# Performance work log

Measured on AMD Instinct MI355X. Metric: run time of the kernel, lower is better.

## Reference

```python
import jax, jax.numpy as jnp
import numpy as np

D_MODEL = 1024
HEADS = 16
D_K = D_MODEL // HEADS

def setup_inputs() -> dict:
    key = jax.random.key(0)
    ks = jax.random.split(key, 12)
    B, S = 4, 2048
    sc = 1.0 / np.sqrt(D_MODEL)
    inp = {
        'q': jax.random.normal(ks[0], (B, S, D_MODEL), jnp.float32),
        'k': jax.random.normal(ks[1], (B, S, D_MODEL), jnp.float32),
        'v': jax.random.normal(ks[2], (B, S, D_MODEL), jnp.float32),
        'mask': jnp.ones((B, S, S), jnp.int32),
        'Wq': jax.random.normal(ks[3], (D_MODEL, D_MODEL), jnp.float32) * sc,
        'bq': jnp.zeros((D_MODEL,), jnp.float32),
        'Wk': jax.random.normal(ks[4], (D_MODEL, D_MODEL), jnp.float32) * sc,
        'bk': jnp.zeros((D_MODEL,), jnp.float32),
        'Wv': jax.random.normal(ks[5], (D_MODEL, D_MODEL), jnp.float32) * sc,
        'bv': jnp.zeros((D_MODEL,), jnp.float32),
        'Wo': jax.random.normal(ks[6], (D_MODEL, D_MODEL), jnp.float32) * sc,
        'bo': jnp.zeros((D_MODEL,), jnp.float32),
    }
    return inp

def _proj_heads(x, W, b):
    # torch Linear: y = x @ W.T + b; then view(B,S,h,dk).transpose(1,2) -> [B,h,S,dk]
    B, S, _ = x.shape
    y = jnp.einsum('bsd,ed->bse', x, W) + b
    return y.reshape(B, S, HEADS, D_K).transpose(0, 2, 1, 3)

def reference(q, k, v, mask, Wq, bq, Wk, bk, Wv, bv, Wo, bo):
    B, S, _ = q.shape
    qh = _proj_heads(q, Wq, bq)  # [B,h,S,dk]
    kh = _proj_heads(k, Wk, bk)
    vh = _proj_heads(v, Wv, bv)
    scores = jnp.einsum('bhqd,bhkd->bhqk', qh, kh) / np.sqrt(D_K)
    scores = jnp.where(mask[:, None, :, :] == 0, jnp.float32(-1e9), scores)
    probs = jax.nn.softmax(scores, axis=-1)  # dropout = identity (eval mode)
    ctx = jnp.einsum('bhqk,bhkd->bhqd', probs, vh)
    concat = ctx.transpose(0, 2, 1, 3).reshape(B, S, D_MODEL)
    return jnp.einsum('bsd,ed->bse', concat, Wo) + bo
```

## Files before the change

kernel.cpp:

```cpp
#include <hip/hip_runtime.h>
#include <stdint.h>

#define DM 1024
#define SQL 2048
#define NB 4
#define NH 16
#define DK 64

typedef unsigned short u16;
typedef unsigned int u32;
typedef float f32x4 __attribute__((ext_vector_type(4)));
typedef short s16x8 __attribute__((ext_vector_type(8)));
typedef unsigned int u32x2 __attribute__((ext_vector_type(2)));

__device__ __forceinline__ u16 f2bf(float x) {
  union { float f; u32 u; } un; un.f = x;
  return (u16)((un.u + 0x8000u) >> 16);
}
__device__ __forceinline__ u32 pack_bf16(float a, float b) {
  return (u32)f2bf(a) | ((u32)f2bf(b) << 16);
}

typedef __attribute__((address_space(3))) u32 lds_u32_t;
typedef __attribute__((address_space(1))) u32 g_u32_t;

__device__ __forceinline__ void async_cp16(void* lds, const void* g) {
  __builtin_amdgcn_global_load_lds((g_u32_t*)(unsigned long long)g,
                                   (lds_u32_t*)(unsigned long long)lds,
                                   16, 0, 0);
}

__device__ __forceinline__ void mfma16(f32x4& c, s16x8 a, s16x8 b) {
  c = __builtin_amdgcn_mfma_f32_16x16x32_bf16(a, b, c, 0, 0, 0);
}

__global__ void init_flag_k(int* flag) { if (threadIdx.x == 0) *flag = 1; }

__device__ __forceinline__ void store_bf4(u16* dst, float4 v) {
  u32 lo = pack_bf16(v.x, v.y);
  u32 hi = pack_bf16(v.z, v.w);
  ((u32*)dst)[0] = lo; ((u32*)dst)[1] = hi;
}

__global__ void __launch_bounds__(256) convert_scan_k(
    const float* __restrict__ q, const float* __restrict__ k, const float* __restrict__ v,
    const float* __restrict__ wq, const float* __restrict__ wk,
    const float* __restrict__ wv, const float* __restrict__ wo,
    const int* __restrict__ mask,
    u16* qb, u16* kb, u16* vb, u16* wqb, u16* wkb, u16* wvb, u16* wob, int* flag)
{
  const size_t i = (size_t)blockIdx.x * 256 + threadIdx.x;
  const size_t i4 = i * 4;
  store_bf4(qb + i4, *(const float4*)(q + i4));
  store_bf4(kb + i4, *(const float4*)(k + i4));
  store_bf4(vb + i4, *(const float4*)(v + i4));
  if (i4 < 1048576) {
    store_bf4(wqb + i4, *(const float4*)(wq + i4));
    store_bf4(wkb + i4, *(const float4*)(wk + i4));
    store_bf4(wvb + i4, *(const float4*)(wv + i4));
    store_bf4(wob + i4, *(const float4*)(wo + i4));
  }
  const size_t mi = i * 8;
  int4 m0 = *(const int4*)(mask + mi);
  int4 m1 = *(const int4*)(mask + mi + 4);
  bool z = (m0.x == 0) | (m0.y == 0) | (m0.z == 0) | (m0.w == 0) |
           (m1.x == 0) | (m1.y == 0) | (m1.z == 0) | (m1.w == 0);
  if (z) *flag = 0;
}

__device__ __forceinline__ void gemm_core(const u16* __restrict__ A, const u16* __restrict__ W,
                                          int m0, int n0, u16* sA, u16* sB, f32x4 (&acc)[4][4])
{
  const int tid = threadIdx.x;
  const int l = tid & 63, w = tid >> 6;
  const int g = l >> 4, ln = l & 15;
  const int wm = w & 1, wn = w >> 1;

  for (int kt = 0; kt < DM; kt += 64) {
#pragma unroll
    for (int i = 0; i < 4; ++i) {
      int s = w * 256 + i * 64 + l;
      int m = s >> 3;
      int kc = (s & 7) ^ (m & 7);
      async_cp16(sA + (size_t)(w * 256 + i * 64) * 8,
                 A + (size_t)(m0 + m) * DM + kt + kc * 8);
    }
#pragma unroll
    for (int i = 0; i < 4; ++i) {
      int s = w * 256 + i * 64 + l;
      int n = s >> 3;
      int kc = (s & 7) ^ (n & 7);
      async_cp16(sB + (size_t)(w * 256 + i * 64) * 8,
                 W + (size_t)(n0 + n) * DM + kt + kc * 8);
    }
    asm volatile("s_waitcnt vmcnt(0)" ::: "memory");
    __syncthreads();
#pragma unroll
    for (int ks = 0; ks < 2; ++ks) {
      s16x8 af[4], bfr[4];
#pragma unroll
      for (int mt = 0; mt < 4; ++mt) {
        int m = wm * 64 + mt * 16 + ln;
        int slot = m * 8 + ((ks * 4 + g) ^ (m & 7));
        af[mt] = *(const s16x8*)(sA + (size_t)slot * 8);
      }
#pragma unroll
      for (int nt = 0; nt < 4; ++nt) {
        int n = wn * 64 + nt * 16 + ln;
        int slot = n * 8 + ((ks * 4 + g) ^ (n & 7));
        bfr[nt] = *(const s16x8*)(sB + (size_t)slot * 8);
      }
#pragma unroll
      for (int mt = 0; mt < 4; ++mt)
#pragma unroll
        for (int nt = 0; nt < 4; ++nt)
          mfma16(acc[mt][nt], af[mt], bfr[nt]);
    }
    __syncthreads();
  }
}

__global__ void __launch_bounds__(256) gemm_qkv_k(
    const u16* __restrict__ qb, const u16* __restrict__ kb, const u16* __restrict__ vb,
    const u16* __restrict__ wqb, const u16* __restrict__ wkb, const u16* __restrict__ wvb,
    const float* __restrict__ bq, const float* __restrict__ bk, const float* __restrict__ bv,
    u16* Qh, u16* Kh, u16* Vt)
{
  __shared__ __align__(16) u16 sA[128 * 64];
  __shared__ __align__(16) u16 sB[128 * 64];
  const int z = blockIdx.z;
  const u16* A = (z == 0) ? qb : ((z == 1) ? kb : vb);
  const u16* W = (z == 0) ? wqb : ((z == 1) ? wkb : wvb);
  const float* bias = (z == 0) ? bq : ((z == 1) ? bk : bv);
  const int m0 = blockIdx.y * 128, n0 = blockIdx.x * 128;

  f32x4 zero4 = {0.f, 0.f, 0.f, 0.f};
  f32x4 acc[4][4];
#pragma unroll
  for (int mt = 0; mt < 4; ++mt)
#pragma unroll
    for (int nt = 0; nt < 4; ++nt) acc[mt][nt] = zero4;

  gemm_core(A, W, m0, n0, sA, sB, acc);

  const int tid = threadIdx.x;
  const int l = tid & 63, w = tid >> 6, g = l >> 4, ln = l & 15;
  const int wm = w & 1, wn = w >> 1;
  const float scale = (z == 0) ? (0.125f * 1.44269504089f) : 1.0f;
  u16* Crow = (z == 0) ? Qh : Kh;
#pragma unroll
  for (int nt = 0; nt < 4; ++nt) {
    int n = n0 + wn * 64 + nt * 16 + ln;
    float bn = bias[n];
#pragma unroll
    for (int mt = 0; mt < 4; ++mt) {
      int mb = m0 + wm * 64 + mt * 16 + g * 4;
      f32x4 vv = acc[mt][nt];
      if (z < 2) {
#pragma unroll
        for (int r = 0; r < 4; ++r)
          Crow[(size_t)(mb + r) * DM + n] = f2bf((vv[r] + bn) * scale);
      } else {
        int b = mb >> 11, s = mb & 2047;
        u32 lo = pack_bf16(vv[0] + bn, vv[1] + bn);
        u32 hi = pack_bf16(vv[2] + bn, vv[3] + bn);
        u32* dst = (u32*)(Vt + ((size_t)b << 21) + (size_t)n * SQL + s);
        dst[0] = lo; dst[1] = hi;
      }
    }
  }
}

__device__ __forceinline__ void stage_kv(u16* Ks, u16* Vs,
                                         const u16* __restrict__ Kh,
                                         const u16* __restrict__ Vt,
                                         int b, int h, int kv0, int w, int l) {
#pragma unroll
  for (int i = 0; i < 4; ++i) {
    int s = w * 256 + i * 64 + l;
    int m = s >> 3;
    int kc = (s & 7) ^ (m & 7);
    async_cp16(Ks + (size_t)(w * 256 + i * 64) * 8,
               Kh + (size_t)(b * SQL + kv0 + m) * DM + h * DK + kc * 8);
  }
#pragma unroll
  for (int i = 0; i < 4; ++i) {
    int s = w * 256 + i * 64 + l;
    int d = s >> 4;
    int kc = (s & 15) ^ (d & 15);
    async_cp16(Vs + (size_t)(w * 256 + i * 64) * 8,
               Vt + ((size_t)b << 21) + (size_t)(h * DK + d) * SQL + kv0 + kc * 8);
  }
}

__device__ __forceinline__ s16x8 p_transpose(u32 x0, u32 x1, u32 y0, u32 y1,
                                             const int LA, const int LB, bool ghi) {
  union { u32 wds[4]; s16x8 v; } pu;
#if __has_builtin(__builtin_amdgcn_permlane32_swap) && __has_builtin(__builtin_amdgcn_permlane16_swap)
  u32x2 r0 = __builtin_amdgcn_permlane32_swap(x0, y0, false, false);
  u32x2 s0 = __builtin_amdgcn_permlane16_swap(r0.x, r0.y, false, false);
  u32x2 r1 = __builtin_amdgcn_permlane32_swap(x1, y1, false, false);
  u32x2 s1 = __builtin_amdgcn_permlane16_swap(r1.x, r1.y, false, false);
  pu.wds[0] = s0.x; pu.wds[1] = s1.x; pu.wds[2] = s0.y; pu.wds[3] = s1.y;
#else
  u32 a0 = __shfl(x0, LA, 64), a1 = __shfl(x1, LA, 64);
  u32 b0 = __shfl(x0, LB, 64), b1 = __shfl(x1, LB, 64);
  u32 c0 = __shfl(y0, LA, 64), c1 = __shfl(y1, LA, 64);
  u32 d0 = __shfl(y0, LB, 64), d1 = __shfl(y1, LB, 64);
  pu.wds[0] = ghi ? c0 : a0;
  pu.wds[1] = ghi ? c1 : a1;
  pu.wds[2] = ghi ? d0 : b0;
  pu.wds[3] = ghi ? d1 : b1;
#endif
  return pu.v;
}

__global__ void __launch_bounds__(256, 2) attn_k(
    const u16* __restrict__ Qh, const u16* __restrict__ Kh, const u16* __restrict__ Vt,
    const int* __restrict__ mask, const int* __restrict__ flag, u16* __restrict__ ctx)
{
  __shared__ __align__(16) u16 smem[32768];
  const int tid = threadIdx.x;
  const int l = tid & 63, w = tid >> 6, g = l >> 4, ln = l & 15;
  const int wq = w >> 1, wk = w & 1;
  const int flat = blockIdx.x + 16 * (blockIdx.y + 16 * blockIdx.z);
  const int nid = (flat & 7) * 128 + (flat >> 3);
  const int q0 = (nid & 15) * 128;
  const int bh = nid >> 4;
  const int h = bh & 15, b = bh >> 4;
  const int allones = *flag;

  s16x8 qf[4][2];
#pragma unroll
  for (int u = 0; u < 4; ++u)
#pragma unroll
    for (int ks = 0; ks < 2; ++ks) {
      size_t row = (size_t)(b * SQL + q0 + wq * 64 + u * 16 + ln);
      qf[u][ks] = *(const s16x8*)(Qh + row * DM + h * DK + ks * 32 + g * 8);
    }

  f32x4 zero4 = {0.f, 0.f, 0.f, 0.f};
  f32x4 ot[4][4];
#pragma unroll
  for (int mt = 0; mt < 4; ++mt)
#pragma unroll
    for (int u = 0; u < 4; ++u) ot[mt][u] = zero4;
  float lsum[4] = {0.f, 0.f, 0.f, 0.f};

  const int LA = (g & 1) * 32 + ln;
  const int LB = LA + 16;
  const bool ghi = (g >> 1) != 0;

  stage_kv(smem, smem + 8192, Kh, Vt, b, h, 0, w, l);

  for (int t = 0; t < 16; ++t) {
    const int kv0 = t * 128;
    u16* Ks = smem + (t & 1) * 16384;
    u16* Vs = smem + 8192 + (t & 1) * 16384;
    if (t < 15) {
      stage_kv(smem + ((t + 1) & 1) * 16384, smem + 8192 + ((t + 1) & 1) * 16384,
               Kh, Vt, b, h, kv0 + 128, w, l);
      asm volatile("s_waitcnt vmcnt(8)" ::: "memory");
    } else {
      asm volatile("s_waitcnt vmcnt(0)" ::: "memory");
    }
    asm volatile("s_barrier" ::: "memory");

#pragma unroll
    for (int kc = 0; kc < 2; ++kc) {
      f32x4 st[2][4];
#pragma unroll
      for (int t2 = 0; t2 < 2; ++t2)
#pragma unroll
        for (int u = 0; u < 4; ++u) st[t2][u] = zero4;
#pragma unroll
      for (int ks = 0; ks < 2; ++ks) {
#pragma unroll
        for (int t2 = 0; t2 < 2; ++t2) {
          int m = wk * 64 + (kc * 2 + t2) * 16 + ln;
          int slot = m * 8 + ((ks * 4 + g) ^ (m & 7));
          s16x8 kf = *(const s16x8*)(Ks + (size_t)slot * 8);
#pragma unroll
          for (int u = 0; u < 4; ++u) mfma16(st[t2][u], kf, qf[u][ks]);
        }
      }

      if (!allones) {
        const int* mb_ = mask + (size_t)b * SQL * SQL;
#pragma unroll
        for (int t2 = 0; t2 < 2; ++t2)
#pragma unroll
          for (int u = 0; u < 4; ++u)
#pragma unroll
            for (int r = 0; r < 4; ++r) {
              int kv = kv0 + wk * 64 + (kc * 2 + t2) * 16 + g * 4 + r;
              int qq = q0 + wq * 64 + u * 16 + ln;
              if (mb_[(size_t)qq * SQL + kv] == 0) st[t2][u][r] = -30.f;
            }
      }

#pragma unroll
      for (int u = 0; u < 4; ++u) {
        u32 pkw[2][2];
#pragma unroll
        for (int t2 = 0; t2 < 2; ++t2) {
          float p0 = __builtin_amdgcn_exp2f(st[t2][u][0]);
          float p1 = __builtin_amdgcn_exp2f(st[t2][u][1]);
          float p2 = __builtin_amdgcn_exp2f(st[t2][u][2]);
          float p3 = __builtin_amdgcn_exp2f(st[t2][u][3]);
          lsum[u] += (p0 + p1) + (p2 + p3);
          pkw[t2][0] = pack_bf16(p0, p1);
          pkw[t2][1] = pack_bf16(p2, p3);
        }
        s16x8 pf = p_transpose(pkw[0][0], pkw[0][1], pkw[1][0], pkw[1][1], LA, LB, ghi);
#pragma unroll
        for (int mt = 0; mt < 4; ++mt) {
          int d = mt * 16 + ln;
          int slot = d * 16 + ((wk * 8 + kc * 4 + g) ^ (d & 15));
          s16x8 vf = *(const s16x8*)(Vs + (size_t)slot * 8);
          mfma16(ot[mt][u], vf, pf);
        }
      }
    }

    asm volatile("s_waitcnt lgkmcnt(0)" ::: "memory");
    asm volatile("s_barrier" ::: "memory");
  }

#pragma unroll
  for (int u = 0; u < 4; ++u) {
    lsum[u] += __shfl_xor(lsum[u], 16, 64);
    lsum[u] += __shfl_xor(lsum[u], 32, 64);
  }

  float* red = (float*)smem;
  __syncthreads();
  if (wk == 1) {
#pragma unroll
    for (int u = 0; u < 4; ++u) {
      int row = wq * 64 + u * 16 + ln;
#pragma unroll
      for (int mt = 0; mt < 4; ++mt)
        *(f32x4*)&red[(size_t)row * 68 + mt * 16 + g * 4] = ot[mt][u];
      if (g == 0) red[(size_t)row * 68 + 64] = lsum[u];
    }
  }
  __syncthreads();
  if (wk == 0) {
#pragma unroll
    for (int u = 0; u < 4; ++u) {
      int row = wq * 64 + u * 16 + ln;
#pragma unroll
      for (int mt = 0; mt < 4; ++mt)
        ot[mt][u] += *(const f32x4*)&red[(size_t)row * 68 + mt * 16 + g * 4];
      lsum[u] += red[(size_t)row * 68 + 64];
    }
  }
  __syncthreads();
  if (wk == 0) {
#pragma unroll
    for (int u = 0; u < 4; ++u) {
      float inv = 1.0f / lsum[u];
      int row = wq * 64 + u * 16 + ln;
#pragma unroll
      for (int mt = 0; mt < 4; ++mt)
#pragma unroll
        for (int r = 0; r < 4; ++r)
          red[(size_t)row * 68 + mt * 16 + g * 4 + r] = ot[mt][u][r] * inv;
    }
  }
  __syncthreads();
#pragma unroll
  for (int i = 0; i < 16; ++i) {
    int f2 = i * 256 + tid;
    int qq = f2 >> 5, dp = f2 & 31;
    float2 vv = *(const float2*)&red[(size_t)qq * 68 + dp * 2];
    u32 pkd = pack_bf16(vv.x, vv.y);
    *(u32*)(ctx + (size_t)(b * SQL + q0 + qq) * DM + h * DK + dp * 2) = pkd;
  }
}

__global__ void __launch_bounds__(256) gemm_out_k(
    const u16* __restrict__ ctx, const u16* __restrict__ wob,
    const float* __restrict__ bo, float* __restrict__ out)
{
  __shared__ __align__(16) u16 sA[128 * 64];
  __shared__ __align__(16) u16 sB[128 * 64];
  const int m0 = blockIdx.y * 128, n0 = blockIdx.x * 128;
  f32x4 zero4 = {0.f, 0.f, 0.f, 0.f};
  f32x4 acc[4][4];
#pragma unroll
  for (int mt = 0; mt < 4; ++mt)
#pragma unroll
    for (int nt = 0; nt < 4; ++nt) acc[mt][nt] = zero4;

  gemm_core(ctx, wob, m0, n0, sA, sB, acc);

  const int tid = threadIdx.x;
  const int l = tid & 63, w = tid >> 6, g = l >> 4, ln = l & 15;
  const int wm = w & 1, wn = w >> 1;
#pragma unroll
  for (int nt = 0; nt < 4; ++nt) {
    int n = n0 + wn * 64 + nt * 16 + ln;
    float bn = bo[n];
#pragma unroll
    for (int mt = 0; mt < 4; ++mt) {
      int mb = m0 + wm * 64 + mt * 16 + g * 4;
      f32x4 vv = acc[mt][nt];
#pragma unroll
      for (int r = 0; r < 4; ++r)
        out[(size_t)(mb + r) * DM + n] = vv[r] + bn;
    }
  }
}

extern "C" void kernel_launch(void* const* d_in, const int* in_sizes, int n_in,
                              void* d_out, int out_size, void* d_ws, size_t ws_size,
                              hipStream_t stream) {
  (void)in_sizes; (void)n_in; (void)out_size; (void)ws_size;
  const float* q  = (const float*)d_in[0];
  const float* k  = (const float*)d_in[1];
  const float* v  = (const float*)d_in[2];
  const int* mask = (const int*)d_in[3];
  const float* Wq = (const float*)d_in[4];
  const float* bq = (const float*)d_in[5];
  const float* Wk = (const float*)d_in[6];
  const float* bk = (const float*)d_in[7];
  const float* Wv = (const float*)d_in[8];
  const float* bv = (const float*)d_in[9];
  const float* Wo = (const float*)d_in[10];
  const float* bo = (const float*)d_in[11];
  float* out = (float*)d_out;
  char* ws = (char*)d_ws;

  u16* qb  = (u16*)(ws + 0);
  u16* kb  = (u16*)(ws + 16777216);
  u16* vb  = (u16*)(ws + 33554432);
  u16* Qh  = (u16*)(ws + 50331648);
  u16* Kh  = (u16*)(ws + 67108864);
  u16* Vt  = (u16*)(ws + 83886080);
  u16* ctx = (u16*)(ws + 100663296);
  u16* wqb = (u16*)(ws + 117440512);
  u16* wkb = (u16*)(ws + 119537664);
  u16* wvb = (u16*)(ws + 121634816);
  u16* wob = (u16*)(ws + 123731968);
  int* flag = (int*)(ws + 125829120);

  hipLaunchKernelGGL(init_flag_k, dim3(1), dim3(64), 0, stream, flag);
  hipLaunchKernelGGL(convert_scan_k, dim3(8192), dim3(256), 0, stream,
                     q, k, v, Wq, Wk, Wv, Wo, mask,
                     qb, kb, vb, wqb, wkb, wvb, wob, flag);
  hipLaunchKernelGGL(gemm_qkv_k, dim3(8, 64, 3), dim3(256), 0, stream,
                     qb, kb, vb, wqb, wkb, wvb, bq, bk, bv, Qh, Kh, Vt);
  hipLaunchKernelGGL(attn_k, dim3(16, 16, 4), dim3(256), 0, stream,
                     Qh, Kh, Vt, mask, flag, ctx);
  hipLaunchKernelGGL(gemm_out_k, dim3(8, 64), dim3(256), 0, stream,
                     ctx, wob, bo, out);
}
```

Measured before the change: 404.6 us.

## Shrink attention KV tile to 64 and drop split-KV warp reduction

The attention kernel now stages 64-key K/V tiles instead of 128 and gives each of the four warps 32 distinct query rows, so warps no longer split the key range. This removes the end-of-kernel cross-warp LDS reduction of partial outputs and sums, and halves per-warp accumulator registers and LDS use so launch bounds can request 4 blocks per CU. The cost is twice as many loop iterations with a full __syncthreads each, and a simpler wait scheme (full barrier instead of vmcnt-based partial waits) that may expose more load latency.

```diff
diff --git a/kernel.cpp b/kernel.cpp
--- a/kernel.cpp
+++ b/kernel.cpp
@@ -176,19 +176,19 @@
                                          const u16* __restrict__ Vt,
                                          int b, int h, int kv0, int w, int l) {
 #pragma unroll
-  for (int i = 0; i < 4; ++i) {
-    int s = w * 256 + i * 64 + l;
+  for (int i = 0; i < 2; ++i) {
+    int s = w * 128 + i * 64 + l;
     int m = s >> 3;
     int kc = (s & 7) ^ (m & 7);
-    async_cp16(Ks + (size_t)(w * 256 + i * 64) * 8,
+    async_cp16(Ks + (size_t)(w * 128 + i * 64) * 8,
                Kh + (size_t)(b * SQL + kv0 + m) * DM + h * DK + kc * 8);
   }
 #pragma unroll
-  for (int i = 0; i < 4; ++i) {
-    int s = w * 256 + i * 64 + l;
-    int d = s >> 4;
-    int kc = (s & 15) ^ (d & 15);
-    async_cp16(Vs + (size_t)(w * 256 + i * 64) * 8,
+  for (int i = 0; i < 2; ++i) {
+    int s = w * 128 + i * 64 + l;
+    int d = s >> 3;
+    int kc = (s & 7) ^ (d & 7);
+    async_cp16(Vs + (size_t)(w * 128 + i * 64) * 8,
                Vt + ((size_t)b << 21) + (size_t)(h * DK + d) * SQL + kv0 + kc * 8);
   }
 }
@@ -215,14 +215,13 @@
   return pu.v;
 }
 
-__global__ void __launch_bounds__(256, 2) attn_k(
+__global__ void __launch_bounds__(256, 4) attn_k(
     const u16* __restrict__ Qh, const u16* __restrict__ Kh, const u16* __restrict__ Vt,
     const int* __restrict__ mask, const int* __restrict__ flag, u16* __restrict__ ctx)
 {
-  __shared__ __align__(16) u16 smem[32768];
+  __shared__ __align__(16) u16 smem[17408];
   const int tid = threadIdx.x;
   const int l = tid & 63, w = tid >> 6, g = l >> 4, ln = l & 15;
-  const int wq = w >> 1, wk = w & 1;
   const int flat = blockIdx.x + 16 * (blockIdx.y + 16 * blockIdx.z);
   const int nid = (flat & 7) * 128 + (flat >> 3);
   const int q0 = (nid & 15) * 128;
@@ -230,58 +229,55 @@
   const int h = bh & 15, b = bh >> 4;
   const int allones = *flag;
 
-  s16x8 qf[4][2];
-#pragma unroll
-  for (int u = 0; u < 4; ++u)
+  s16x8 qf[2][2];
+#pragma unroll
+  for (int u = 0; u < 2; ++u)
 #pragma unroll
     for (int ks = 0; ks < 2; ++ks) {
-      size_t row = (size_t)(b * SQL + q0 + wq * 64 + u * 16 + ln);
+      size_t row = (size_t)(b * SQL + q0 + w * 32 + u * 16 + ln);
       qf[u][ks] = *(const s16x8*)(Qh + row * DM + h * DK + ks * 32 + g * 8);
     }
 
   f32x4 zero4 = {0.f, 0.f, 0.f, 0.f};
-  f32x4 ot[4][4];
+  f32x4 ot[4][2];
 #pragma unroll
   for (int mt = 0; mt < 4; ++mt)
 #pragma unroll
-    for (int u = 0; u < 4; ++u) ot[mt][u] = zero4;
-  float lsum[4] = {0.f, 0.f, 0.f, 0.f};
+    for (int u = 0; u < 2; ++u) ot[mt][u] = zero4;
+  float lsum[2] = {0.f, 0.f};
 
   const int LA = (g & 1) * 32 + ln;
   const int LB = LA + 16;
   const bool ghi = (g >> 1) != 0;
 
-  stage_kv(smem, smem + 8192, Kh, Vt, b, h, 0, w, l);
-
-  for (int t = 0; t < 16; ++t) {
-    const int kv0 = t * 128;
-    u16* Ks = smem + (t & 1) * 16384;
-    u16* Vs = smem + 8192 + (t & 1) * 16384;
-    if (t < 15) {
-      stage_kv(smem + ((t + 1) & 1) * 16384, smem + 8192 + ((t + 1) & 1) * 16384,
-               Kh, Vt, b, h, kv0 + 128, w, l);
-      asm volatile("s_waitcnt vmcnt(8)" ::: "memory");
-    } else {
-      asm volatile("s_waitcnt vmcnt(0)" ::: "memory");
-    }
-    asm volatile("s_barrier" ::: "memory");
+  stage_kv(smem, smem + 4096, Kh, Vt, b, h, 0, w, l);
+  __syncthreads();
+
+  for (int t = 0; t < 32; ++t) {
+    const int kv0 = t * 64;
+    u16* Ks = smem + (t & 1) * 8192;
+    u16* Vs = Ks + 4096;
+    if (t < 31) {
+      u16* Kn = smem + ((t + 1) & 1) * 8192;
+      stage_kv(Kn, Kn + 4096, Kh, Vt, b, h, kv0 + 64, w, l);
+    }
 
 #pragma unroll
     for (int kc = 0; kc < 2; ++kc) {
-      f32x4 st[2][4];
+      f32x4 st[2][2];
 #pragma unroll
       for (int t2 = 0; t2 < 2; ++t2)
 #pragma unroll
-        for (int u = 0; u < 4; ++u) st[t2][u] = zero4;
+        for (int u = 0; u < 2; ++u) st[t2][u] = zero4;
 #pragma unroll
       for (int ks = 0; ks < 2; ++ks) {
 #pragma unroll
         for (int t2 = 0; t2 < 2; ++t2) {
-          int m = wk * 64 + (kc * 2 + t2) * 16 + ln;
+          int m = kc * 32 + t2 * 16 + ln;
           int slot = m * 8 + ((ks * 4 + g) ^ (m & 7));
           s16x8 kf = *(const s16x8*)(Ks + (size_t)slot * 8);
 #pragma unroll
-          for (int u = 0; u < 4; ++u) mfma16(st[t2][u], kf, qf[u][ks]);
+          for (int u = 0; u < 2; ++u) mfma16(st[t2][u], kf, qf[u][ks]);
         }
       }
 
@@ -290,17 +286,17 @@
 #pragma unroll
         for (int t2 = 0; t2 < 2; ++t2)
 #pragma unroll
-          for (int u = 0; u < 4; ++u)
+          for (int u = 0; u < 2; ++u)
 #pragma unroll
             for (int r = 0; r < 4; ++r) {
-              int kv = kv0 + wk * 64 + (kc * 2 + t2) * 16 + g * 4 + r;
-              int qq = q0 + wq * 64 + u * 16 + ln;
+              int kv = kv0 + kc * 32 + t2 * 16 + g * 4 + r;
+              int qq = q0 + w * 32 + u * 16 + ln;
               if (mb_[(size_t)qq * SQL + kv] == 0) st[t2][u][r] = -30.f;
             }
       }
 
 #pragma unroll
-      for (int u = 0; u < 4; ++u) {
+      for (int u = 0; u < 2; ++u) {
         u32 pkw[2][2];
 #pragma unroll
         for (int t2 = 0; t2 < 2; ++t2) {
@@ -316,57 +312,31 @@
 #pragma unroll
         for (int mt = 0; mt < 4; ++mt) {
           int d = mt * 16 + ln;
-          int slot = d * 16 + ((wk * 8 + kc * 4 + g) ^ (d & 15));
+          int slot = d * 8 + ((kc * 4 + g) ^ (d & 7));
           s16x8 vf = *(const s16x8*)(Vs + (size_t)slot * 8);
           mfma16(ot[mt][u], vf, pf);
         }
       }
     }
 
-    asm volatile("s_waitcnt lgkmcnt(0)" ::: "memory");
-    asm volatile("s_barrier" ::: "memory");
-  }
-
-#pragma unroll
-  for (int u = 0; u < 4; ++u) {
+    __syncthreads();
+  }
+
+#pragma unroll
+  for (int u = 0; u < 2; ++u) {
     lsum[u] += __shfl_xor(lsum[u], 16, 64);
     lsum[u] += __shfl_xor(lsum[u], 32, 64);
   }
 
   float* red = (float*)smem;
-  __syncthreads();
-  if (wk == 1) {
-#pragma unroll
-    for (int u = 0; u < 4; ++u) {
-      int row = wq * 64 + u * 16 + ln;
-#pragma unroll
-      for (int mt = 0; mt < 4; ++mt)
-        *(f32x4*)&red[(size_t)row * 68 + mt * 16 + g * 4] = ot[mt][u];
-      if (g == 0) red[(size_t)row * 68 + 64] = lsum[u];
-    }
-  }
-  __syncthreads();
-  if (wk == 0) {
-#pragma unroll
-    for (int u = 0; u < 4; ++u) {
-      int row = wq * 64 + u * 16 + ln;
-#pragma unroll
-      for (int mt = 0; mt < 4; ++mt)
-        ot[mt][u] += *(const f32x4*)&red[(size_t)row * 68 + mt * 16 + g * 4];
-      lsum[u] += red[(size_t)row * 68 + 64];
-    }
-  }
-  __syncthreads();
-  if (wk == 0) {
-#pragma unroll
-    for (int u = 0; u < 4; ++u) {
-      float inv = 1.0f / lsum[u];
-      int row = wq * 64 + u * 16 + ln;
-#pragma unroll
-      for (int mt = 0; mt < 4; ++mt)
-#pragma unroll
-        for (int r = 0; r < 4; ++r)
-          red[(size_t)row * 68 + mt * 16 + g * 4 + r] = ot[mt][u][r] * inv;
+#pragma unroll
+  for (int u = 0; u < 2; ++u) {
+    float inv = 1.0f / lsum[u];
+    int row = w * 32 + u * 16 + ln;
+#pragma unroll
+    for (int mt = 0; mt < 4; ++mt) {
+      f32x4 vv = ot[mt][u] * inv;
+      *(f32x4*)&red[(size_t)row * 68 + mt * 16 + g * 4] = vv;
     }
   }
   __syncthreads();
```

After: 400.5 us. No clear change (-1.0%).
